# Kernel tuning notes

Measured on AMD Instinct MI355X. Metric: run time of the kernel, lower is better.

Reference implementation:

```python
import jax, jax.numpy as jnp
import numpy as np

B, N, D, H = 2, 2048, 1024, 16
DH = D // H
MASK_VALUE = -1e7


def setup_inputs() -> dict:
    key = jax.random.key(0)
    ks = jax.random.split(key, 8)
    scale = 0.02
    return {
        "queries": jax.random.normal(ks[0], (B, N, D), dtype=jnp.float32),
        "keys": jax.random.normal(ks[1], (B, N, D), dtype=jnp.float32),
        "values": jax.random.normal(ks[2], (B, N, D), dtype=jnp.float32),
        "valid_len": jax.random.randint(ks[3], (B * H,), 1, N + 1, dtype=jnp.int32),
        "Wq": jax.random.normal(ks[4], (D, D), dtype=jnp.float32) * scale,
        "Wk": jax.random.normal(ks[5], (D, D), dtype=jnp.float32) * scale,
        "Wv": jax.random.normal(ks[6], (D, D), dtype=jnp.float32) * scale,
        "Wo": jax.random.normal(ks[7], (D, D), dtype=jnp.float32) * scale,
    }


def reference(queries, keys, values, valid_len, Wq, Wk, Wv, Wo):
    b, n, d = queries.shape
    h, dh = H, d // H

    def split_heads(x):  # (b, n, d) -> (b, h, n, dh)
        return x.reshape(b, n, h, dh).transpose(0, 2, 1, 3)

    q = split_heads(queries @ Wq)
    k = split_heads(keys @ Wk)
    v = split_heads(values @ Wv)

    # (b, h, nq, nk) full score tensor, as in the original naive bmm path
    scores = jnp.einsum("bhqd,bhkd->bhqk", q, k) / jnp.sqrt(jnp.float32(dh))

    # valid_len is 1-D of length b*h; repeat_interleave over queries means the
    # mask depends only on the key index: keep k < valid_len[bh]
    vl = valid_len.reshape(b, h, 1, 1)
    keep = jnp.arange(n)[None, None, None, :] < vl  # (b, h, 1, nk)
    scores = jnp.where(keep, scores, MASK_VALUE)

    attn = jax.nn.softmax(scores, axis=-1)
    heads = jnp.einsum("bhqk,bhkd->bhqd", attn, v)  # (b, h, n, dh)
    out = heads.transpose(0, 2, 1, 3).reshape(b, n, d) @ Wo
    return out
```

## Files before the change

### kernel.cpp

```cpp
#include <hip/hip_runtime.h>

#define B_ 2
#define N_ 2048
#define D_ 1024
#define H_ 16
#define DH_ 64
#define NITEMS 1024

typedef _Float16 half8 __attribute__((ext_vector_type(8)));
typedef _Float16 half4 __attribute__((ext_vector_type(4)));
typedef float f32x4 __attribute__((ext_vector_type(4)));

__device__ __forceinline__ void gl2lds16(const _Float16* g, _Float16* l) {
  __builtin_amdgcn_global_load_lds(
      (const __attribute__((address_space(1))) void*)g,
      (__attribute__((address_space(3))) void*)l, 16, 0, 0);
}

__global__ __launch_bounds__(256) void prep_kernel(
    const float* __restrict__ q, const float* __restrict__ k,
    const float* __restrict__ v, const float* __restrict__ Wq,
    const float* __restrict__ Wk, const float* __restrict__ Wv,
    const float* __restrict__ Wo, const int* __restrict__ vlen,
    _Float16* __restrict__ Xf, _Float16* __restrict__ WtAll,
    int* __restrict__ order) {
  __shared__ float tile[64][65];
  const int bid = blockIdx.x;
  if (bid < 6144) {
    int y = bid >> 11, x = bid & 2047;
    const float* s = (y == 0) ? q : (y == 1) ? k : v;
    _Float16* d = Xf + (size_t)y * ((size_t)B_ * N_ * D_);
    size_t idx = ((size_t)x * 256 + threadIdx.x) * 8;
    float4 a = *(const float4*)(s + idx);
    float4 b = *(const float4*)(s + idx + 4);
    half8 h;
    h[0] = (_Float16)a.x; h[1] = (_Float16)a.y; h[2] = (_Float16)a.z; h[3] = (_Float16)a.w;
    h[4] = (_Float16)b.x; h[5] = (_Float16)b.y; h[6] = (_Float16)b.z; h[7] = (_Float16)b.w;
    *(half8*)(d + idx) = h;
  } else if (bid < 6144 + 1024) {
    int idx = bid - 6144;
    int z = idx >> 8, rem = idx & 255, gy = rem >> 4, gx = rem & 15;
    const float* W = (z == 0) ? Wq : (z == 1) ? Wk : (z == 2) ? Wv : Wo;
    _Float16* Wt = WtAll + (size_t)z * D_ * D_;
    int k0 = gy * 64, n0 = gx * 64;
    int tr = threadIdx.x >> 4, tc = threadIdx.x & 15;
#pragma unroll
    for (int i = 0; i < 4; ++i) {
      int r = tr + i * 16;
      float4 va = *(const float4*)(W + (size_t)(k0 + r) * D_ + n0 + tc * 4);
      tile[r][tc * 4 + 0] = va.x; tile[r][tc * 4 + 1] = va.y;
      tile[r][tc * 4 + 2] = va.z; tile[r][tc * 4 + 3] = va.w;
    }
    __syncthreads();
#pragma unroll
    for (int i = 0; i < 4; ++i) {
      int r = tr + i * 16;
      half4 hv;
      hv[0] = (_Float16)tile[tc * 4 + 0][r];
      hv[1] = (_Float16)tile[tc * 4 + 1][r];
      hv[2] = (_Float16)tile[tc * 4 + 2][r];
      hv[3] = (_Float16)tile[tc * 4 + 3][r];
      *(half4*)(Wt + (size_t)(n0 + r) * D_ + k0 + tc * 4) = hv;
    }
  } else {
    int i = threadIdx.x;
    if (i < B_ * H_) {
      int vi = vlen[i], rank = 0;
      for (int j = 0; j < B_ * H_; ++j) {
        int vj = vlen[j];
        if (vj > vi || (vj == vi && j < i)) ++rank;
      }
      order[rank] = i;
    }
  }
}

#define BK 32

template <int NT, int MODE>
__global__ __launch_bounds__(256) void gemm_f16_kernel(
    const _Float16* __restrict__ Aall, const _Float16* __restrict__ Btall,
    _Float16* __restrict__ ChAll, float* __restrict__ Cf32) {
  constexpr int BN = NT * 32;
  constexpr int K = D_;
  __shared__ __attribute__((aligned(16))) _Float16 As[128 * BK];
  __shared__ __attribute__((aligned(16))) _Float16 Bs[BN * BK];
  const int z = blockIdx.z;
  const _Float16* A  = Aall  + (size_t)z * ((size_t)B_ * N_ * D_);
  const _Float16* Bt = Btall + (size_t)z * ((size_t)D_ * D_);
  _Float16* Chead = ChAll + (size_t)z * ((size_t)B_ * N_ * D_);

  const int tid = threadIdx.x;
  const int m0 = blockIdx.y * 128, n0 = blockIdx.x * BN;
  const int lane = tid & 63, w = tid >> 6;
  const int quad = lane >> 4, l15 = lane & 15;
  const int wm = (w >> 1) * 64, wn = (w & 1) * (BN / 2);
  const int swz = (quad ^ ((l15 >> 1) & 3)) * 8;
  f32x4 acc[4][NT] = {};

  for (int kt = 0; kt < K; kt += BK) {
    if (kt) __syncthreads();
#pragma unroll
    for (int p = 0; p < 2; ++p) {
      int c = p * 256 + tid;
      int row = c >> 2, pg = c & 3;
      int gl = pg ^ ((row >> 1) & 3);
      gl2lds16(A + (size_t)(m0 + row) * K + kt + gl * 8, &As[c * 8]);
    }
#pragma unroll
    for (int p = 0; p < NT / 2; ++p) {
      int c = p * 256 + tid;
      int row = c >> 2, pg = c & 3;
      int gl = pg ^ ((row >> 1) & 3);
      gl2lds16(Bt + (size_t)(n0 + row) * K + kt + gl * 8, &Bs[c * 8]);
    }
    __syncthreads();
    half8 af[4], bf[NT];
#pragma unroll
    for (int mt = 0; mt < 4; ++mt)
      af[mt] = *(const half8*)&As[(wm + mt * 16 + l15) * 32 + swz];
#pragma unroll
    for (int nt = 0; nt < NT; ++nt)
      bf[nt] = *(const half8*)&Bs[(wn + nt * 16 + l15) * 32 + swz];
#pragma unroll
    for (int mt = 0; mt < 4; ++mt)
#pragma unroll
      for (int nt = 0; nt < NT; ++nt)
        acc[mt][nt] = __builtin_amdgcn_mfma_f32_16x16x32_f16(
            af[mt], bf[nt], acc[mt][nt], 0, 0, 0);
  }

#pragma unroll
  for (int mt = 0; mt < 4; ++mt) {
    int mrow = m0 + wm + mt * 16 + quad * 4;
#pragma unroll
    for (int nt = 0; nt < NT; ++nt) {
      int jcol = n0 + wn + nt * 16 + l15;
      if (MODE == 0) {
        int b = mrow >> 11, n = mrow & (N_ - 1);
        int h = jcol >> 6, dh = jcol & (DH_ - 1);
        if (z == 2) {
          half4 o;
#pragma unroll
          for (int r = 0; r < 4; ++r) o[r] = (_Float16)acc[mt][nt][r];
          *(half4*)(ChAll + 2 * (size_t)B_ * N_ * D_ +
                    ((size_t)(b * H_ + h) * DH_ + dh) * N_ + n) = o;
        } else {
#pragma unroll
          for (int r = 0; r < 4; ++r)
            Chead[((((size_t)(b * H_ + h)) * N_ + n + r) * DH_) + dh] =
                (_Float16)acc[mt][nt][r];
        }
      } else {
#pragma unroll
        for (int r = 0; r < 4; ++r)
          Cf32[(size_t)(mrow + r) * D_ + jcol] = acc[mt][nt][r];
      }
    }
  }
}

__global__ __launch_bounds__(256, 4) void attn_kernel(
    const _Float16* __restrict__ Qh, const _Float16* __restrict__ Kh,
    const _Float16* __restrict__ VtG, const int* __restrict__ vlen,
    _Float16* __restrict__ Hd, const int* __restrict__ order) {
  __shared__ __attribute__((aligned(16))) _Float16 Ks[2][64 * 64];
  __shared__ __attribute__((aligned(16))) _Float16 Vt[2][64 * 64];
  const int tid = threadIdx.x, lane = tid & 63, w = tid >> 6;
  const int quad = lane >> 4, l15 = lane & 15;
  const int sw  = (quad ^ (l15 & 7)) * 8;
  const int sw2 = ((quad + 4) ^ (l15 & 7)) * 8;
  const float sc2 = 0.125f * 1.44269504088896f;
  const half4 ones = {(_Float16)1, (_Float16)1, (_Float16)1, (_Float16)1};

  const int bid = blockIdx.x;
  const int xcd = bid & 7;
  const int wi  = bid >> 3;
  const int i4 = wi & 3, t = wi >> 2;
  const int qsel = (i4 + t + (t >> 3)) & 3;
  const int rank = xcd + 8 * qsel;
  const int bh = order[rank];
  const int q0 = t * 64;
  const int b = bh >> 4, h = bh & (H_ - 1);
  const int vl = vlen[bh];
  const int KT = (vl + 63) >> 6;
  const _Float16* Qb = Qh  + (size_t)bh * N_ * DH_;
  const _Float16* Kb = Kh  + (size_t)bh * N_ * DH_;
  const _Float16* Vb = VtG + (size_t)bh * N_ * DH_;

  const half8 qb0 = *(const half8*)(Qb + (size_t)(q0 + w * 16 + l15) * DH_ + quad * 8);
  const half8 qb1 = *(const half8*)(Qb + (size_t)(q0 + w * 16 + l15) * DH_ + 32 + quad * 8);

  half8 kpre[2], vpre[2];
  auto prefetch = [&](int k0k) {
#pragma unroll
    for (int p = 0; p < 2; ++p) {
      int c = p * 256 + tid;
      int row = c >> 3, pg = c & 7;
      kpre[p] = *(const half8*)(Kb + (size_t)(k0k + row) * DH_ + (pg ^ (row & 7)) * 8);
      vpre[p] = *(const half8*)(Vb + (size_t)row * N_ + k0k + pg * 8);
    }
  };
  auto commit = [&](int buf) {
#pragma unroll
    for (int p = 0; p < 2; ++p) {
      int c = p * 256 + tid;
      int row = c >> 3, pg = c & 7;
      *(half8*)&Ks[buf][c * 8] = kpre[p];
      int j0 = (pg * 2) ^ (row & 15), j1 = (pg * 2 + 1) ^ (row & 15);
      half4 lo = {vpre[p][0], vpre[p][1], vpre[p][2], vpre[p][3]};
      half4 hi = {vpre[p][4], vpre[p][5], vpre[p][6], vpre[p][7]};
      *(half4*)&Vt[buf][row * 64 + j0 * 4] = lo;
      *(half4*)&Vt[buf][row * 64 + j1 * 4] = hi;
    }
  };

  prefetch(0);
  commit(0);
  if (KT > 1) prefetch(64);
  __syncthreads();

  f32x4 Oacc[4] = {};
  f32x4 lacc = {};

  for (int kt = 0; kt < KT; ++kt) {
    const int cur = kt & 1;
    if (kt + 1 < KT) commit(1 - cur);
    if (kt + 2 < KT) prefetch((kt + 2) * 64);

    f32x4 s[4];
#pragma unroll
    for (int nt = 0; nt < 4; ++nt) {
      int r = nt * 16 + l15;
      half8 ka0 = *(const half8*)&Ks[cur][r * 64 + sw];
      half8 ka1 = *(const half8*)&Ks[cur][r * 64 + sw2];
      f32x4 c = {};
      c = __builtin_amdgcn_mfma_f32_16x16x32_f16(ka0, qb0, c, 0, 0, 0);
      c = __builtin_amdgcn_mfma_f32_16x16x32_f16(ka1, qb1, c, 0, 0, 0);
      s[nt] = c;
    }
    const int k0k = kt * 64;
    half4 pf[4];
    if (k0k + 64 <= vl) {
#pragma unroll
      for (int nt = 0; nt < 4; ++nt)
#pragma unroll
        for (int r = 0; r < 4; ++r)
          pf[nt][r] = (_Float16)exp2f(s[nt][r] * sc2);
    } else {
#pragma unroll
      for (int nt = 0; nt < 4; ++nt) {
        int keyb = k0k + nt * 16 + quad * 4;
#pragma unroll
        for (int r = 0; r < 4; ++r) {
          float p = exp2f(s[nt][r] * sc2);
          pf[nt][r] = (keyb + r < vl) ? (_Float16)p : (_Float16)0.f;
        }
      }
    }
#pragma unroll
    for (int nt = 0; nt < 4; ++nt) {
      lacc = __builtin_amdgcn_mfma_f32_16x16x16f16(ones, pf[nt], lacc, 0, 0, 0);
#pragma unroll
      for (int dt = 0; dt < 4; ++dt) {
        int dh = dt * 16 + l15;
        half4 va = *(const half4*)&Vt[cur][dh * 64 + (((nt * 4 + quad) ^ l15) << 2)];
        Oacc[dt] = __builtin_amdgcn_mfma_f32_16x16x16f16(va, pf[nt], Oacc[dt], 0, 0, 0);
      }
    }
    __syncthreads();
  }

  float inv_l = 1.0f / lacc[0];
  int q = q0 + w * 16 + l15;
  _Float16* out = Hd + ((size_t)(b * N_ + q)) * D_ + h * DH_;
#pragma unroll
  for (int dt = 0; dt < 4; ++dt) {
    half4 o;
#pragma unroll
    for (int r = 0; r < 4; ++r) o[r] = (_Float16)(Oacc[dt][r] * inv_l);
    *(half4*)(out + dt * 16 + quad * 4) = o;
  }
}

extern "C" void kernel_launch(void* const* d_in, const int* in_sizes, int n_in,
                              void* d_out, int out_size, void* d_ws, size_t ws_size,
                              hipStream_t stream) {
  const float* q  = (const float*)d_in[0];
  const float* k  = (const float*)d_in[1];
  const float* v  = (const float*)d_in[2];
  const int*   vl = (const int*)d_in[3];
  const float* Wq = (const float*)d_in[4];
  const float* Wk = (const float*)d_in[5];
  const float* Wv = (const float*)d_in[6];
  const float* Wo = (const float*)d_in[7];

  const size_t XSZ = (size_t)B_ * N_ * D_;
  const size_t WSZ = (size_t)D_ * D_;
  _Float16* ws = (_Float16*)d_ws;
  _Float16* Xf = ws;
  _Float16* Wt = Xf + 3 * XSZ;
  _Float16* Qh = Wt + 4 * WSZ;
  _Float16* Hd = Qh + 3 * XSZ;
  int* order = (int*)(Hd + XSZ);

  prep_kernel<<<dim3(6144 + 1024 + 1), 256, 0, stream>>>(
      q, k, v, Wq, Wk, Wv, Wo, vl, Xf, Wt, order);

  gemm_f16_kernel<4, 0><<<dim3(D_ / 128, 32, 3), 256, 0, stream>>>(
      Xf, Wt, Qh, nullptr);

  attn_kernel<<<dim3(NITEMS), 256, 0, stream>>>(
      Qh, Qh + XSZ, Qh + 2 * XSZ, vl, Hd, order);

  gemm_f16_kernel<2, 1><<<dim3(D_ / 64, 32, 1), 256, 0, stream>>>(
      Hd, Wt + 3 * WSZ, nullptr, (float*)d_out);
}
```

Before: 222.2 us.

## Make attention kernel persistent with atomic work queue over vlen-sorted items

The attention kernel changes from one block per (head, query-tile) item, with a static XCD-aware mapping, to 768 persistent blocks. Each block repeatedly claims the next item from a global atomic counter, which is reset in the prep kernel. Items are taken in order of decreasing valid length, so the longest heads are scheduled first and the rest balance dynamically. The cost is an atomic and an extra barrier per item, and the loss of the previous XCD-locality-aware placement of heads.

```diff
diff --git a/kernel.cpp b/kernel.cpp
--- a/kernel.cpp
+++ b/kernel.cpp
@@ -23,7 +23,7 @@
     const float* __restrict__ Wk, const float* __restrict__ Wv,
     const float* __restrict__ Wo, const int* __restrict__ vlen,
     _Float16* __restrict__ Xf, _Float16* __restrict__ WtAll,
-    int* __restrict__ order) {
+    int* __restrict__ order, int* __restrict__ qctr) {
   __shared__ float tile[64][65];
   const int bid = blockIdx.x;
   if (bid < 6144) {
@@ -64,6 +64,7 @@
     }
   } else {
     int i = threadIdx.x;
+    if (i == 0) *qctr = 0;
     if (i < B_ * H_) {
       int vi = vlen[i], rank = 0;
       for (int j = 0; j < B_ * H_; ++j) {
@@ -163,9 +164,11 @@
 __global__ __launch_bounds__(256, 4) void attn_kernel(
     const _Float16* __restrict__ Qh, const _Float16* __restrict__ Kh,
     const _Float16* __restrict__ VtG, const int* __restrict__ vlen,
-    _Float16* __restrict__ Hd, const int* __restrict__ order) {
+    _Float16* __restrict__ Hd, const int* __restrict__ order,
+    int* __restrict__ qctr) {
   __shared__ __attribute__((aligned(16))) _Float16 Ks[2][64 * 64];
   __shared__ __attribute__((aligned(16))) _Float16 Vt[2][64 * 64];
+  __shared__ int sIt;
   const int tid = threadIdx.x, lane = tid & 63, w = tid >> 6;
   const int quad = lane >> 4, l15 = lane & 15;
   const int sw  = (quad ^ (l15 & 7)) * 8;
@@ -173,113 +176,114 @@
   const float sc2 = 0.125f * 1.44269504088896f;
   const half4 ones = {(_Float16)1, (_Float16)1, (_Float16)1, (_Float16)1};
 
-  const int bid = blockIdx.x;
-  const int xcd = bid & 7;
-  const int wi  = bid >> 3;
-  const int i4 = wi & 3, t = wi >> 2;
-  const int qsel = (i4 + t + (t >> 3)) & 3;
-  const int rank = xcd + 8 * qsel;
-  const int bh = order[rank];
-  const int q0 = t * 64;
-  const int b = bh >> 4, h = bh & (H_ - 1);
-  const int vl = vlen[bh];
-  const int KT = (vl + 63) >> 6;
-  const _Float16* Qb = Qh  + (size_t)bh * N_ * DH_;
-  const _Float16* Kb = Kh  + (size_t)bh * N_ * DH_;
-  const _Float16* Vb = VtG + (size_t)bh * N_ * DH_;
-
-  const half8 qb0 = *(const half8*)(Qb + (size_t)(q0 + w * 16 + l15) * DH_ + quad * 8);
-  const half8 qb1 = *(const half8*)(Qb + (size_t)(q0 + w * 16 + l15) * DH_ + 32 + quad * 8);
-
-  half8 kpre[2], vpre[2];
-  auto prefetch = [&](int k0k) {
-#pragma unroll
-    for (int p = 0; p < 2; ++p) {
-      int c = p * 256 + tid;
-      int row = c >> 3, pg = c & 7;
-      kpre[p] = *(const half8*)(Kb + (size_t)(k0k + row) * DH_ + (pg ^ (row & 7)) * 8);
-      vpre[p] = *(const half8*)(Vb + (size_t)row * N_ + k0k + pg * 8);
-    }
-  };
-  auto commit = [&](int buf) {
-#pragma unroll
-    for (int p = 0; p < 2; ++p) {
-      int c = p * 256 + tid;
-      int row = c >> 3, pg = c & 7;
-      *(half8*)&Ks[buf][c * 8] = kpre[p];
-      int j0 = (pg * 2) ^ (row & 15), j1 = (pg * 2 + 1) ^ (row & 15);
-      half4 lo = {vpre[p][0], vpre[p][1], vpre[p][2], vpre[p][3]};
-      half4 hi = {vpre[p][4], vpre[p][5], vpre[p][6], vpre[p][7]};
-      *(half4*)&Vt[buf][row * 64 + j0 * 4] = lo;
-      *(half4*)&Vt[buf][row * 64 + j1 * 4] = hi;
-    }
-  };
-
-  prefetch(0);
-  commit(0);
-  if (KT > 1) prefetch(64);
-  __syncthreads();
-
-  f32x4 Oacc[4] = {};
-  f32x4 lacc = {};
-
-  for (int kt = 0; kt < KT; ++kt) {
-    const int cur = kt & 1;
-    if (kt + 1 < KT) commit(1 - cur);
-    if (kt + 2 < KT) prefetch((kt + 2) * 64);
-
-    f32x4 s[4];
-#pragma unroll
-    for (int nt = 0; nt < 4; ++nt) {
-      int r = nt * 16 + l15;
-      half8 ka0 = *(const half8*)&Ks[cur][r * 64 + sw];
-      half8 ka1 = *(const half8*)&Ks[cur][r * 64 + sw2];
-      f32x4 c = {};
-      c = __builtin_amdgcn_mfma_f32_16x16x32_f16(ka0, qb0, c, 0, 0, 0);
-      c = __builtin_amdgcn_mfma_f32_16x16x32_f16(ka1, qb1, c, 0, 0, 0);
-      s[nt] = c;
-    }
-    const int k0k = kt * 64;
-    half4 pf[4];
-    if (k0k + 64 <= vl) {
-#pragma unroll
-      for (int nt = 0; nt < 4; ++nt)
-#pragma unroll
-        for (int r = 0; r < 4; ++r)
-          pf[nt][r] = (_Float16)exp2f(s[nt][r] * sc2);
-    } else {
+  for (;;) {
+    if (tid == 0) sIt = atomicAdd(qctr, 1);
+    __syncthreads();
+    const int item = sIt;
+    if (item >= NITEMS) break;
+
+    const int bh = order[item >> 5];
+    const int q0 = (item & 31) * 64;
+    const int b = bh >> 4, h = bh & (H_ - 1);
+    const int vl = vlen[bh];
+    const int KT = (vl + 63) >> 6;
+    const _Float16* Qb = Qh  + (size_t)bh * N_ * DH_;
+    const _Float16* Kb = Kh  + (size_t)bh * N_ * DH_;
+    const _Float16* Vb = VtG + (size_t)bh * N_ * DH_;
+
+    const half8 qb0 = *(const half8*)(Qb + (size_t)(q0 + w * 16 + l15) * DH_ + quad * 8);
+    const half8 qb1 = *(const half8*)(Qb + (size_t)(q0 + w * 16 + l15) * DH_ + 32 + quad * 8);
+
+    half8 kpre[2], vpre[2];
+    auto prefetch = [&](int k0k) {
+#pragma unroll
+      for (int p = 0; p < 2; ++p) {
+        int c = p * 256 + tid;
+        int row = c >> 3, pg = c & 7;
+        kpre[p] = *(const half8*)(Kb + (size_t)(k0k + row) * DH_ + (pg ^ (row & 7)) * 8);
+        vpre[p] = *(const half8*)(Vb + (size_t)row * N_ + k0k + pg * 8);
+      }
+    };
+    auto commit = [&](int buf) {
+#pragma unroll
+      for (int p = 0; p < 2; ++p) {
+        int c = p * 256 + tid;
+        int row = c >> 3, pg = c & 7;
+        *(half8*)&Ks[buf][c * 8] = kpre[p];
+        int j0 = (pg * 2) ^ (row & 15), j1 = (pg * 2 + 1) ^ (row & 15);
+        half4 lo = {vpre[p][0], vpre[p][1], vpre[p][2], vpre[p][3]};
+        half4 hi = {vpre[p][4], vpre[p][5], vpre[p][6], vpre[p][7]};
+        *(half4*)&Vt[buf][row * 64 + j0 * 4] = lo;
+        *(half4*)&Vt[buf][row * 64 + j1 * 4] = hi;
+      }
+    };
+
+    prefetch(0);
+    commit(0);
+    if (KT > 1) prefetch(64);
+    __syncthreads();
+
+    f32x4 Oacc[4] = {};
+    f32x4 lacc = {};
+
+    for (int kt = 0; kt < KT; ++kt) {
+      const int cur = kt & 1;
+      if (kt + 1 < KT) commit(1 - cur);
+      if (kt + 2 < KT) prefetch((kt + 2) * 64);
+
+      f32x4 s[4];
 #pragma unroll
       for (int nt = 0; nt < 4; ++nt) {
-        int keyb = k0k + nt * 16 + quad * 4;
-#pragma unroll
-        for (int r = 0; r < 4; ++r) {
-          float p = exp2f(s[nt][r] * sc2);
-          pf[nt][r] = (keyb + r < vl) ? (_Float16)p : (_Float16)0.f;
+        int r = nt * 16 + l15;
+        half8 ka0 = *(const half8*)&Ks[cur][r * 64 + sw];
+        half8 ka1 = *(const half8*)&Ks[cur][r * 64 + sw2];
+        f32x4 c = {};
+        c = __builtin_amdgcn_mfma_f32_16x16x32_f16(ka0, qb0, c, 0, 0, 0);
+        c = __builtin_amdgcn_mfma_f32_16x16x32_f16(ka1, qb1, c, 0, 0, 0);
+        s[nt] = c;
+      }
+      const int k0k = kt * 64;
+      half4 pf[4];
+      if (k0k + 64 <= vl) {
+#pragma unroll
+        for (int nt = 0; nt < 4; ++nt)
+#pragma unroll
+          for (int r = 0; r < 4; ++r)
+            pf[nt][r] = (_Float16)exp2f(s[nt][r] * sc2);
+      } else {
+#pragma unroll
+        for (int nt = 0; nt < 4; ++nt) {
+          int keyb = k0k + nt * 16 + quad * 4;
+#pragma unroll
+          for (int r = 0; r < 4; ++r) {
+            float p = exp2f(s[nt][r] * sc2);
+            pf[nt][r] = (keyb + r < vl) ? (_Float16)p : (_Float16)0.f;
+          }
         }
       }
-    }
-#pragma unroll
-    for (int nt = 0; nt < 4; ++nt) {
-      lacc = __builtin_amdgcn_mfma_f32_16x16x16f16(ones, pf[nt], lacc, 0, 0, 0);
-#pragma unroll
-      for (int dt = 0; dt < 4; ++dt) {
-        int dh = dt * 16 + l15;
-        half4 va = *(const half4*)&Vt[cur][dh * 64 + (((nt * 4 + quad) ^ l15) << 2)];
-        Oacc[dt] = __builtin_amdgcn_mfma_f32_16x16x16f16(va, pf[nt], Oacc[dt], 0, 0, 0);
-      }
-    }
-    __syncthreads();
-  }
-
-  float inv_l = 1.0f / lacc[0];
-  int q = q0 + w * 16 + l15;
-  _Float16* out = Hd + ((size_t)(b * N_ + q)) * D_ + h * DH_;
-#pragma unroll
-  for (int dt = 0; dt < 4; ++dt) {
-    half4 o;
-#pragma unroll
-    for (int r = 0; r < 4; ++r) o[r] = (_Float16)(Oacc[dt][r] * inv_l);
-    *(half4*)(out + dt * 16 + quad * 4) = o;
+#pragma unroll
+      for (int nt = 0; nt < 4; ++nt) {
+        lacc = __builtin_amdgcn_mfma_f32_16x16x16f16(ones, pf[nt], lacc, 0, 0, 0);
+#pragma unroll
+        for (int dt = 0; dt < 4; ++dt) {
+          int dh = dt * 16 + l15;
+          half4 va = *(const half4*)&Vt[cur][dh * 64 + (((nt * 4 + quad) ^ l15) << 2)];
+          Oacc[dt] = __builtin_amdgcn_mfma_f32_16x16x16f16(va, pf[nt], Oacc[dt], 0, 0, 0);
+        }
+      }
+      __syncthreads();
+    }
+
+    float inv_l = 1.0f / lacc[0];
+    int q = q0 + w * 16 + l15;
+    _Float16* out = Hd + ((size_t)(b * N_ + q)) * D_ + h * DH_;
+#pragma unroll
+    for (int dt = 0; dt < 4; ++dt) {
+      half4 o;
+#pragma unroll
+      for (int r = 0; r < 4; ++r) o[r] = (_Float16)(Oacc[dt][r] * inv_l);
+      *(half4*)(out + dt * 16 + quad * 4) = o;
+    }
   }
 }
 
@@ -303,15 +307,16 @@
   _Float16* Qh = Wt + 4 * WSZ;
   _Float16* Hd = Qh + 3 * XSZ;
   int* order = (int*)(Hd + XSZ);
+  int* qctr  = order + 32;
 
   prep_kernel<<<dim3(6144 + 1024 + 1), 256, 0, stream>>>(
-      q, k, v, Wq, Wk, Wv, Wo, vl, Xf, Wt, order);
+      q, k, v, Wq, Wk, Wv, Wo, vl, Xf, Wt, order, qctr);
 
   gemm_f16_kernel<4, 0><<<dim3(D_ / 128, 32, 3), 256, 0, stream>>>(
       Xf, Wt, Qh, nullptr);
 
-  attn_kernel<<<dim3(NITEMS), 256, 0, stream>>>(
-      Qh, Qh + XSZ, Qh + 2 * XSZ, vl, Hd, order);
+  attn_kernel<<<dim3(768), 256, 0, stream>>>(
+      Qh, Qh + XSZ, Qh + 2 * XSZ, vl, Hd, order, qctr);
 
   gemm_f16_kernel<2, 1><<<dim3(D_ / 64, 32, 1), 256, 0, stream>>>(
       Hd, Wt + 3 * WSZ, nullptr, (float*)d_out);
```

Result: slower. 229.1 us (+3.1%).
